# Performance work log

Hardware: AMD Instinct MI355X
Metric: run time of the kernel (lower is better)

## Reference

```python
import jax, jax.numpy as jnp
import numpy as np

DIM = 2048
N_HEADS = 16
N_KV_HEADS = 8
HEAD_DIM = DIM // N_HEADS  # 128
N_REP = N_HEADS // N_KV_HEADS
THETA = 10000.0


def _rope_cos_sin(seq_len, head_dim):
    # freqs_cis = polar(1, outer(t, 1/theta^(2i/d))), i in [0, head_dim//2)
    inv = 1.0 / (THETA ** (jnp.arange(0, head_dim, 2, dtype=jnp.float32) / head_dim))
    t = jnp.arange(seq_len, dtype=jnp.float32)
    freqs = jnp.outer(t, inv)  # [S, hd/2]
    return jnp.cos(freqs), jnp.sin(freqs)


def _apply_rope(x, cos, sin):
    # x: [B, S, H, hd]; pairs (even, odd) treated as complex and multiplied by e^{i*freq}
    xr = x[..., 0::2]
    xi = x[..., 1::2]
    c = cos[None, :, None, :]
    s = sin[None, :, None, :]
    out_r = xr * c - xi * s
    out_i = xr * s + xi * c
    return jnp.stack([out_r, out_i], axis=-1).reshape(x.shape)


def setup_inputs() -> dict:
    key = jax.random.key(0)
    ks = jax.random.split(key, 5)
    B, S = 2, 2048
    sc = 0.02
    return {
        "x": jax.random.normal(ks[0], (B, S, DIM), dtype=jnp.float32),
        "wq": jax.random.normal(ks[1], (N_HEADS * HEAD_DIM, DIM), dtype=jnp.float32) * sc,
        "wk": jax.random.normal(ks[2], (N_KV_HEADS * HEAD_DIM, DIM), dtype=jnp.float32) * sc,
        "wv": jax.random.normal(ks[3], (N_KV_HEADS * HEAD_DIM, DIM), dtype=jnp.float32) * sc,
        "wo": jax.random.normal(ks[4], (DIM, N_HEADS * HEAD_DIM), dtype=jnp.float32) * sc,
        "start_pos": 0,
        "inference": 0,
    }


def reference(x, wq, wk, wv, wo, start_pos, inference):
    B, S, _ = x.shape
    xq = (x @ wq.T).reshape(B, S, N_HEADS, HEAD_DIM)
    xk = (x @ wk.T).reshape(B, S, N_KV_HEADS, HEAD_DIM)
    xv = (x @ wv.T).reshape(B, S, N_KV_HEADS, HEAD_DIM)

    cos, sin = _rope_cos_sin(S, HEAD_DIM)
    xq = _apply_rope(xq, cos, sin)
    xk = _apply_rope(xk, cos, sin)

    # repeat_kv (GQA): [B,S,Hkv,hd] -> [B,S,Hkv*n_rep,hd]
    xk = jnp.repeat(xk, N_REP, axis=2)
    xv = jnp.repeat(xv, N_REP, axis=2)

    q = xq.transpose(0, 2, 1, 3)  # [B,H,S,hd]
    k = xk.transpose(0, 2, 1, 3)
    v = xv.transpose(0, 2, 1, 3)

    scores = jnp.einsum("bhqd,bhkd->bhqk", q, k) / np.sqrt(HEAD_DIM).astype(np.float32)
    mask = jnp.triu(jnp.full((S, S), -jnp.inf, dtype=scores.dtype), k=1)
    scores = scores + mask
    probs = jax.nn.softmax(scores.astype(jnp.float32), axis=-1).astype(q.dtype)

    out = jnp.einsum("bhqk,bhkd->bhqd", probs, v)
    out = out.transpose(0, 2, 1, 3).reshape(B, S, N_HEADS * HEAD_DIM)
    return out @ wo.T
```

## Files before the change

kernel.cpp:

```cpp
#include <hip/hip_runtime.h>
#include <hip/hip_bf16.h>
#include <stdint.h>
#include <type_traits>

typedef __attribute__((ext_vector_type(4))) float   f32x4;
typedef __attribute__((ext_vector_type(8))) __bf16  bf16x8;
typedef __attribute__((ext_vector_type(4))) unsigned int u32x4;

#define B_   2
#define S_   2048
#define DIM_ 2048
#define NH_  16
#define NKV_ 8
#define HD_  128

__device__ inline unsigned short f2bf(float f) {
    unsigned u = __float_as_uint(f);
    unsigned r = (u + 0x7fffu + ((u >> 16) & 1u)) >> 16;
    return (unsigned short)r;
}
__device__ inline float bf2f(unsigned short s) {
    return __uint_as_float(((unsigned)s) << 16);
}

__global__ void k_convert(const float* __restrict__ x,  const float* __restrict__ wq,
                          const float* __restrict__ wk, const float* __restrict__ wv,
                          const float* __restrict__ wo,
                          unsigned short* __restrict__ xb,  unsigned short* __restrict__ wqkb,
                          unsigned short* __restrict__ wvb, unsigned short* __restrict__ wob,
                          float* __restrict__ tab)
{
    int i = blockIdx.x * blockDim.x + threadIdx.x;
    const int NX = 2097152, NWQ = 1048576, NWK = 524288, NWV = 524288, NWO = 1048576;
    const int NTOT = NX + NWQ + NWK + NWV + NWO;
    if (i >= NTOT) {
        int t = i - NTOT;
        if (t >= S_ * 64) return;
        int ii = t & 63;
        int s = t >> 6;
        float inv = expf(-((float)ii / 64.0f) * 9.210340371976184f);
        float ang = (float)s * inv;
        tab[2 * t]     = cosf(ang);
        tab[2 * t + 1] = sinf(ang);
        return;
    }
    const float* src; unsigned short* dst; int j = i;
    if (j < NX) { src = x; dst = xb; }
    else {
        j -= NX;
        if (j < NWQ) { src = wq; dst = wqkb; }
        else {
            j -= NWQ;
            if (j < NWK) { src = wk; dst = wqkb + (size_t)2048 * 2048; }
            else {
                j -= NWK;
                if (j < NWV) { src = wv; dst = wvb; }
                else { j -= NWV; src = wo; dst = wob; }
            }
        }
    }
    float4 v = reinterpret_cast<const float4*>(src)[j];
    ushort4 o;
    o.x = f2bf(v.x); o.y = f2bf(v.y); o.z = f2bf(v.z); o.w = f2bf(v.w);
    reinterpret_cast<ushort4*>(dst)[j] = o;
}

#define BAR  __builtin_amdgcn_s_barrier()
#define WLG  asm volatile("s_waitcnt lgkmcnt(0)" ::: "memory")
#define WVM4 asm volatile("s_waitcnt vmcnt(4)" ::: "memory")
#define WVM6 asm volatile("s_waitcnt vmcnt(6)" ::: "memory")
#define WVM0 asm volatile("s_waitcnt vmcnt(0)" ::: "memory")

#define G_LDS(SRC, DST) __builtin_amdgcn_global_load_lds( \
    (const __attribute__((address_space(1))) void*)(SRC), \
    (__attribute__((address_space(3))) void*)(DST), 16, 0, 0)

#define STAGE(MATB, DBUF, HALF, KT) do { \
    const unsigned short* _s0 = ((MATB) ? pb0 : pa0) + (size_t)(HALF) * 128 * 2048 + (KT) * 64; \
    const unsigned short* _s1 = ((MATB) ? pb1 : pa1) + (size_t)(HALF) * 128 * 2048 + (KT) * 64; \
    G_LDS(_s0, lds + (MATB) * 32768 + (DBUF) * 16384 + (HALF) * 8192 + lo0); \
    G_LDS(_s1, lds + (MATB) * 32768 + (DBUF) * 16384 + (HALF) * 8192 + lo1); \
} while (0)

#define LDA(DBUF, MH) { \
    _Pragma("unroll") \
    for (int mf = 0; mf < 4; ++mf) { \
        _Pragma("unroll") \
        for (int kk = 0; kk < 2; ++kk) { \
            const int R = wm * 128 + (MH) * 64 + mf * 16 + lr; \
            afr[MH][mf][kk] = *reinterpret_cast<const bf16x8*>( \
                &lds[(DBUF) * 16384 + R * 64 + (((kk * 4 + g) ^ (lr & 7)) * 8)]); \
        } } }

#define LDB(DBUF, NH) { \
    _Pragma("unroll") \
    for (int nf = 0; nf < 2; ++nf) { \
        _Pragma("unroll") \
        for (int kk = 0; kk < 2; ++kk) { \
            const int R = wn * 64 + (NH) * 32 + nf * 16 + lr; \
            bfr[NH][nf][kk] = *reinterpret_cast<const bf16x8*>( \
                &lds[32768 + (DBUF) * 16384 + R * 64 + (((kk * 4 + g) ^ (lr & 7)) * 8)]); \
        } } }

#define MMA(MH, NH) { \
    __builtin_amdgcn_s_setprio(1); \
    _Pragma("unroll") \
    for (int mf = 0; mf < 4; ++mf) { \
        _Pragma("unroll") \
        for (int nf = 0; nf < 2; ++nf) { \
            _Pragma("unroll") \
            for (int kk = 0; kk < 2; ++kk) \
                acc[(MH) * 4 + mf][(NH) * 2 + nf] = __builtin_amdgcn_mfma_f32_16x16x32_bf16( \
                    afr[MH][mf][kk], bfr[NH][nf][kk], acc[(MH) * 4 + mf][(NH) * 2 + nf], 0, 0, 0); \
        } } \
    __builtin_amdgcn_s_setprio(0); }

__global__ __launch_bounds__(512, 2) void k_gemm_qkv(
    const unsigned short* __restrict__ A0g, const unsigned short* __restrict__ B0g,
    const unsigned short* __restrict__ A1g,
    unsigned short* __restrict__ Cq, unsigned short* __restrict__ Cv,
    const float* __restrict__ tab)
{
    __shared__ __attribute__((aligned(16))) unsigned short lds[65536];

    const int tid  = threadIdx.x;
    const int lane = tid & 63;
    const int wid  = tid >> 6;
    const int g    = lane >> 4;
    const int lr   = lane & 15;
    const int wm   = wid >> 2;
    const int wn   = wid & 3;

    const unsigned short *Ag, *Bg;
    int brow, bcol;
    bool isQK = true;
    {
        int swz = (blockIdx.x & 7) * 32 + (blockIdx.x >> 3);
        if (swz < 192) { Ag = A0g; Bg = B0g; brow = (swz / 12) << 8; bcol = (swz % 12) << 8; }
        else { int ix = swz - 192; isQK = false; Ag = A1g; Bg = A0g; brow = (ix >> 4) << 8; bcol = (ix & 15) << 8; }
    }

    const int E0 = wid * 512 + lane * 8;
    const int E1 = E0 + 4096;
    const int r0 = E0 >> 6, r1 = E1 >> 6;
    const int c0 = ((((E0 >> 3) & 7) ^ (r0 & 7)) * 8);
    const int c1 = ((((E1 >> 3) & 7) ^ (r1 & 7)) * 8);
    const unsigned short* pa0 = Ag + (size_t)(brow + r0) * 2048 + c0;
    const unsigned short* pa1 = Ag + (size_t)(brow + r1) * 2048 + c1;
    const unsigned short* pb0 = Bg + (size_t)(bcol + r0) * 2048 + c0;
    const unsigned short* pb1 = Bg + (size_t)(bcol + r1) * 2048 + c1;
    const int lo0 = wid * 512;
    const int lo1 = lo0 + 4096;

    f32x4 acc[8][4] = {};
    bf16x8 afr[2][4][2];
    bf16x8 bfr[2][2][2];

    STAGE(0, 0, 0, 0); STAGE(0, 0, 1, 0); STAGE(1, 0, 0, 0); STAGE(1, 0, 1, 0);
    STAGE(0, 1, 0, 1); STAGE(1, 1, 0, 1);
    WVM0; BAR;

    #pragma unroll 1
    for (int i = 0; i < 16; ++i) {
        const int kt1 = 2 * i + 1;
        int kt2 = 2 * i + 2;  if (kt2 >= 32) kt2 -= 32;
        int kt3 = 2 * i + 3;  if (kt3 >= 32) kt3 -= 32;
        LDA(0, 0); LDB(0, 0);
        STAGE(0, 1, 1, kt1);
        BAR; WLG; MMA(0, 0); BAR;
        LDA(0, 1);
        STAGE(1, 1, 1, kt1);
        BAR; WLG; MMA(1, 0); BAR;
        LDB(0, 1);
        STAGE(1, 0, 0, kt2);
        BAR; WLG; MMA(0, 1); BAR;
        STAGE(0, 0, 0, kt2);
        WVM4;
        BAR; WLG; MMA(1, 1); BAR;
        LDA(1, 0); LDB(1, 0);
        STAGE(0, 0, 1, kt2);
        BAR; WLG; MMA(0, 0); BAR;
        LDA(1, 1);
        STAGE(1, 0, 1, kt2);
        BAR; WLG; MMA(1, 0); BAR;
        LDB(1, 1);
        STAGE(1, 1, 0, kt3);
        BAR; WLG; MMA(0, 1); BAR;
        STAGE(0, 1, 0, kt3);
        WVM4;
        BAR; WLG; MMA(1, 1); BAR;
    }

    if (isQK) {
        #pragma unroll
        for (int m = 0; m < 8; ++m) {
            #pragma unroll
            for (int n = 0; n < 4; ++n) {
                int col = bcol + wn * 64 + (n >> 1) * 32 + (n & 1) * 16 + lr;
                int ci  = (col & 127) >> 1;
                int row0 = brow + wm * 128 + (m >> 2) * 64 + (m & 3) * 16 + g * 4;
                #pragma unroll
                for (int r = 0; r < 4; ++r) {
                    int row = row0 + r;
                    int s   = row & (S_ - 1);
                    float2 cs = *reinterpret_cast<const float2*>(&tab[(s * 64 + ci) * 2]);
                    float v = acc[m][n][r];
                    float o = __shfl_xor(v, 1);
                    float res = (lane & 1) ? fmaf(o, cs.y, v * cs.x)
                                           : fmaf(v, cs.x, -(o * cs.y));
                    Cq[(size_t)row * 3072 + col] = f2bf(res);
                }
            }
        }
    } else {
        #pragma unroll
        for (int m = 0; m < 8; ++m)
            #pragma unroll
            for (int n = 0; n < 4; ++n)
                #pragma unroll
                for (int r = 0; r < 4; ++r) {
                    int row = brow + wm * 128 + (m >> 2) * 64 + (m & 3) * 16 + g * 4 + r;
                    int col = bcol + wn * 64 + (n >> 1) * 32 + (n & 1) * 16 + lr;
                    Cv[(size_t)row * 4096 + col] = f2bf(acc[m][n][r]);
                }
    }
}

#define OP_LDA(D, MH) { \
    _Pragma("unroll") \
    for (int mf = 0; mf < 2; ++mf) { \
        _Pragma("unroll") \
        for (int kk = 0; kk < 2; ++kk) { \
            const int R = wm * 64 + (MH) * 32 + mf * 16 + lr; \
            afr[mf][kk] = *reinterpret_cast<const bf16x8*>( \
                &lds[(D) * 8192 + R * 64 + (((kk * 4 + g) ^ (lr & 7)) * 8)]); \
        } } }

#define OP_LDB(D, NH, BFR) { \
    _Pragma("unroll") \
    for (int nf = 0; nf < 2; ++nf) { \
        _Pragma("unroll") \
        for (int kk = 0; kk < 2; ++kk) { \
            const int R = wn * 64 + (NH) * 32 + nf * 16 + lr; \
            BFR[nf][kk] = *reinterpret_cast<const bf16x8*>( \
                &lds[16384 + (D) * 16384 + R * 64 + (((kk * 4 + g) ^ (lr & 7)) * 8)]); \
        } } }

#define OP_MMA(MH, NH, BFR) { \
    __builtin_amdgcn_s_setprio(1); \
    _Pragma("unroll") \
    for (int mf = 0; mf < 2; ++mf) { \
        _Pragma("unroll") \
        for (int nf = 0; nf < 2; ++nf) { \
            _Pragma("unroll") \
            for (int kk = 0; kk < 2; ++kk) \
                acc[(MH) * 2 + mf][(NH) * 2 + nf] = __builtin_amdgcn_mfma_f32_16x16x32_bf16( \
                    afr[mf][kk], BFR[nf][kk], acc[(MH) * 2 + mf][(NH) * 2 + nf], 0, 0, 0); \
        } } \
    __builtin_amdgcn_s_setprio(0); }

#define OP_SA(D, KT) do { \
    G_LDS(pa0 + (KT) * 64, lds + (D) * 8192 + t8); \
    G_LDS(pa1 + (KT) * 64, lds + (D) * 8192 + 4096 + t8); \
} while (0)
#define OP_SB01(D, KT) do { \
    G_LDS(pb0 + (KT) * 64, lds + 16384 + (D) * 16384 + t8); \
    G_LDS(pb1 + (KT) * 64, lds + 16384 + (D) * 16384 + 4096 + t8); \
} while (0)
#define OP_SB23(D, KT) do { \
    G_LDS(pb2 + (KT) * 64, lds + 16384 + (D) * 16384 + 8192 + t8); \
    G_LDS(pb3 + (KT) * 64, lds + 16384 + (D) * 16384 + 12288 + t8); \
} while (0)

__global__ __launch_bounds__(512, 1) void k_gemm_op(
    const unsigned short* __restrict__ Ag,
    const unsigned short* __restrict__ Bg,
    float* __restrict__ C)
{
    __shared__ __attribute__((aligned(16))) unsigned short lds[49152];

    const int tid  = threadIdx.x;
    const int lane = tid & 63;
    const int wid  = tid >> 6;
    const int g    = lane >> 4;
    const int lr   = lane & 15;
    const int wm   = wid >> 2;
    const int wn   = wid & 3;

    const int swz  = (blockIdx.x & 7) * 32 + (blockIdx.x >> 3);
    const int brow = (swz >> 3) << 7;
    const int bcol = (swz & 7) << 8;

    const int E = tid * 8;
    const int r = E >> 6;
    const int c = (((E >> 3) & 7) ^ (r & 7)) * 8;
    const int t8 = tid * 8;
    const unsigned short* pa0 = Ag + (size_t)(brow + r)       * 2048 + c;
    const unsigned short* pa1 = Ag + (size_t)(brow + 64 + r)  * 2048 + c;
    const unsigned short* pb0 = Bg + (size_t)(bcol + r)       * 2048 + c;
    const unsigned short* pb1 = Bg + (size_t)(bcol + 64 + r)  * 2048 + c;
    const unsigned short* pb2 = Bg + (size_t)(bcol + 128 + r) * 2048 + c;
    const unsigned short* pb3 = Bg + (size_t)(bcol + 192 + r) * 2048 + c;

    f32x4 acc[4][4] = {};
    bf16x8 afr[2][2];
    bf16x8 bfr0[2][2], bfr1[2][2];

    OP_SA(0, 0); OP_SB01(0, 0); OP_SB23(0, 0);
    OP_SA(1, 1); OP_SB01(1, 1); OP_SB23(1, 1);
    WVM0; BAR;

    #pragma unroll 1
    for (int i = 0; i < 16; ++i) {
        int kt2 = 2 * i + 2;  if (kt2 >= 32) kt2 -= 32;
        int kt3 = 2 * i + 3;  if (kt3 >= 32) kt3 -= 32;
        OP_LDA(0, 0); OP_LDB(0, 0, bfr0);
        BAR; WLG; OP_MMA(0, 0, bfr0); BAR;
        OP_LDB(0, 1, bfr1);
        BAR; WLG; OP_MMA(0, 1, bfr1); BAR;
        OP_LDA(0, 1);
        OP_SB01(0, kt2);
        BAR; WLG; OP_MMA(1, 0, bfr0); BAR;
        OP_SB23(0, kt2); OP_SA(0, kt2);
        WVM6;
        BAR; WLG; OP_MMA(1, 1, bfr1); BAR;
        OP_LDA(1, 0); OP_LDB(1, 0, bfr0);
        BAR; WLG; OP_MMA(0, 0, bfr0); BAR;
        OP_LDB(1, 1, bfr1);
        BAR; WLG; OP_MMA(0, 1, bfr1); BAR;
        OP_LDA(1, 1);
        OP_SB01(1, kt3);
        BAR; WLG; OP_MMA(1, 0, bfr0); BAR;
        OP_SB23(1, kt3); OP_SA(1, kt3);
        WVM6;
        BAR; WLG; OP_MMA(1, 1, bfr1); BAR;
    }

    #pragma unroll
    for (int m = 0; m < 4; ++m)
        #pragma unroll
        for (int n = 0; n < 4; ++n)
            #pragma unroll
            for (int rr = 0; rr < 4; ++rr) {
                int row = brow + wm * 64 + m * 16 + g * 4 + rr;
                int col = bcol + wn * 64 + n * 16 + lr;
                C[(size_t)row * 2048 + col] = acc[m][n][rr];
            }
}

__global__ __launch_bounds__(512, 4) void k_attn(
    const unsigned short* __restrict__ QK,
    const unsigned short* __restrict__ Vt,
    unsigned short* __restrict__ O)
{
    __shared__ __attribute__((aligned(16))) unsigned short Ks[64 * 128];
    __shared__ __attribute__((aligned(16))) unsigned short Vs[128 * 64];

    const int tid  = threadIdx.x;
    const int lane = tid & 63;
    const int wid  = tid >> 6;
    const int g    = lane >> 4;
    const int lr   = lane & 15;

    const int bid  = blockIdx.x;
    const int hk   = bid & 7;
    const int j    = bid >> 3;
    const int p    = j & 1;
    const int cc   = j >> 1;
    const int h    = (hk << 1) | p;
    const int b    = j >> 5;
    const int base = (cc < 16) ? cc : (31 - cc);
    const int qt   = p ? (15 - base) : base;
    const int q0w  = qt * 128 + wid * 16;

    bf16x8 qf[4];
    #pragma unroll
    for (int c = 0; c < 4; ++c)
        qf[c] = *reinterpret_cast<const bf16x8*>(
            QK + (size_t)(b * S_ + q0w + lr) * 3072 + h * HD_ + c * 32 + g * 8);

    f32x4 o_acc[8] = {};
    float m_run = -INFINITY;
    float l_run = 0.f;

    const float C2 = 1.4426950408889634f * 0.08838834764831845f;
    const int nt = 2 * qt + 2;
    const int srcb = (g & 1) * 32 + lr;
    const bool hig = g >> 1;

    #pragma unroll 1
    for (int t = 0; t < nt; ++t) {
        const int kv0 = t * 64;
        __syncthreads();
        #pragma unroll
        for (int i4 = 0; i4 < 2; ++i4) {
            const int base2 = (i4 * 8 + wid) * 512;
            const int E = base2 + lane * 8;
            {
                int row = E >> 7, ch = (E >> 3) & 15;
                int col = ((ch ^ (row & 15)) * 8);
                G_LDS(QK + (size_t)(b * S_ + kv0 + row) * 3072 + 2048 + hk * HD_ + col,
                      &Ks[base2]);
            }
            {
                int d = E >> 6, ch = (E >> 3) & 7;
                int kv = ((ch ^ (d & 7)) * 8);
                G_LDS(Vt + (size_t)(hk * HD_ + d) * (B_ * S_) + b * S_ + kv0 + kv,
                      &Vs[base2]);
            }
        }
        __syncthreads();

        const bool active = kv0 < q0w + 16;
        if (active) {
            f32x4 sv[4] = {};
            __builtin_amdgcn_s_setprio(1);
            #pragma unroll
            for (int c = 0; c < 4; ++c)
                #pragma unroll
                for (int kvb = 0; kvb < 4; ++kvb) {
                    bf16x8 kf = *reinterpret_cast<const bf16x8*>(
                        &Ks[(kvb * 16 + lr) * 128 + (((c * 4 + g) ^ lr) * 8)]);
                    sv[kvb] = __builtin_amdgcn_mfma_f32_16x16x32_bf16(
                        kf, qf[c], sv[kvb], 0, 0, 0);
                }
            __builtin_amdgcn_s_setprio(0);

            if (kv0 + 63 > q0w) {
                int qg = q0w + lr;
                #pragma unroll
                for (int kvb = 0; kvb < 4; ++kvb) {
                    int kvg0 = kv0 + kvb * 16 + g * 4;
                    #pragma unroll
                    for (int r = 0; r < 4; ++r)
                        if (kvg0 + r > qg) sv[kvb][r] = -INFINITY;
                }
            }

            float m0 = fmaxf(fmaxf(fmaxf(sv[0][0], sv[0][1]), fmaxf(sv[0][2], sv[0][3])),
                             fmaxf(fmaxf(sv[1][0], sv[1][1]), fmaxf(sv[1][2], sv[1][3])));
            m0 = fmaxf(m0, fmaxf(fmaxf(sv[2][0], sv[2][1]), fmaxf(sv[2][2], sv[2][3])));
            m0 = fmaxf(m0, fmaxf(fmaxf(sv[3][0], sv[3][1]), fmaxf(sv[3][2], sv[3][3])));
            m0 = fmaxf(m0, __shfl_xor(m0, 16));
            m0 = fmaxf(m0, __shfl_xor(m0, 32));

            if (__any(m0 > m_run + 90.5f)) {
                float mn = fmaxf(m_run, m0);
                float al = exp2f((m_run - mn) * C2);
                m_run = mn;
                l_run *= al;
                #pragma unroll
                for (int db = 0; db < 8; ++db)
                    #pragma unroll
                    for (int r = 0; r < 4; ++r)
                        o_acc[db][r] *= al;
            }

            unsigned pk[4][2];
            float mb2 = m_run * C2;
            float rs = 0.f;
            #pragma unroll
            for (int kvb = 0; kvb < 4; ++kvb) {
                float p0 = exp2f(fmaf(sv[kvb][0], C2, -mb2));
                float p1 = exp2f(fmaf(sv[kvb][1], C2, -mb2));
                float p2 = exp2f(fmaf(sv[kvb][2], C2, -mb2));
                float p3 = exp2f(fmaf(sv[kvb][3], C2, -mb2));
                rs += (p0 + p1) + (p2 + p3);
                pk[kvb][0] = (unsigned)f2bf(p0) | ((unsigned)f2bf(p1) << 16);
                pk[kvb][1] = (unsigned)f2bf(p2) | ((unsigned)f2bf(p3) << 16);
            }
            rs += __shfl_xor(rs, 16);
            rs += __shfl_xor(rs, 32);
            l_run += rs;

            #pragma unroll
            for (int kk = 0; kk < 2; ++kk) {
                u32x4 w;
                unsigned a0 = (unsigned)__shfl((int)pk[2 * kk][0], srcb);
                unsigned a1 = (unsigned)__shfl((int)pk[2 * kk][1], srcb);
                unsigned a2 = (unsigned)__shfl((int)pk[2 * kk][0], srcb + 16);
                unsigned a3 = (unsigned)__shfl((int)pk[2 * kk][1], srcb + 16);
                unsigned b0 = (unsigned)__shfl((int)pk[2 * kk + 1][0], srcb);
                unsigned b1 = (unsigned)__shfl((int)pk[2 * kk + 1][1], srcb);
                unsigned b2 = (unsigned)__shfl((int)pk[2 * kk + 1][0], srcb + 16);
                unsigned b3 = (unsigned)__shfl((int)pk[2 * kk + 1][1], srcb + 16);
                w[0] = hig ? b0 : a0;
                w[1] = hig ? b1 : a1;
                w[2] = hig ? b2 : a2;
                w[3] = hig ? b3 : a3;
                bf16x8 pb = *reinterpret_cast<const bf16x8*>(&w);
                __builtin_amdgcn_s_setprio(1);
                #pragma unroll
                for (int db = 0; db < 8; ++db) {
                    bf16x8 vf = *reinterpret_cast<const bf16x8*>(
                        &Vs[(db * 16 + lr) * 64 + (((kk * 4 + g) ^ (lr & 7)) * 8)]);
                    o_acc[db] = __builtin_amdgcn_mfma_f32_16x16x32_bf16(
                        vf, pb, o_acc[db], 0, 0, 0);
                }
                __builtin_amdgcn_s_setprio(0);
            }
        }
    }

    {
        float inv = 1.f / l_run;
        size_t rowb = ((size_t)(b * S_ + q0w + lr) * NH_ + h) * HD_;
        #pragma unroll
        for (int db = 0; db < 8; ++db) {
            ushort4 o4;
            o4.x = f2bf(o_acc[db][0] * inv);
            o4.y = f2bf(o_acc[db][1] * inv);
            o4.z = f2bf(o_acc[db][2] * inv);
            o4.w = f2bf(o_acc[db][3] * inv);
            *reinterpret_cast<ushort4*>(&O[rowb + db * 16 + g * 4]) = o4;
        }
    }
}

extern "C" void kernel_launch(void* const* d_in, const int* in_sizes, int n_in,
                              void* d_out, int out_size, void* d_ws, size_t ws_size,
                              hipStream_t stream)
{
    const float* x  = (const float*)d_in[0];
    const float* wq = (const float*)d_in[1];
    const float* wk = (const float*)d_in[2];
    const float* wv = (const float*)d_in[3];
    const float* wo = (const float*)d_in[4];
    float* out = (float*)d_out;

    char* ws = (char*)d_ws;
    size_t off = 0;
    auto alloc = [&](size_t bytes) -> void* {
        void* p = ws + off;
        off += (bytes + 255) & ~(size_t)255;
        return p;
    };
    unsigned short* xb   = (unsigned short*)alloc((size_t)B_ * S_ * DIM_ * 2);
    unsigned short* wqkb = (unsigned short*)alloc((size_t)3072 * 2048 * 2);
    unsigned short* wvb  = (unsigned short*)alloc((size_t)1024 * 2048 * 2);
    unsigned short* wob  = (unsigned short*)alloc((size_t)DIM_ * DIM_ * 2);
    unsigned short* QKb  = (unsigned short*)alloc((size_t)B_ * S_ * 3072 * 2);
    unsigned short* Vtb  = (unsigned short*)alloc((size_t)1024 * B_ * S_ * 2);
    unsigned short* Ob   = (unsigned short*)alloc((size_t)B_ * S_ * NH_ * HD_ * 2);
    float* tab = (float*)alloc((size_t)S_ * 64 * 2 * 4);

    k_convert<<<20992, 256, 0, stream>>>(x, wq, wk, wv, wo, xb, wqkb, wvb, wob, tab);
    k_gemm_qkv<<<256, 512, 0, stream>>>(xb, wqkb, wvb, QKb, Vtb, tab);
    k_attn<<<B_ * NH_ * (S_ / 128), 512, 0, stream>>>(QKb, Vtb, Ob);
    k_gemm_op<<<256, 512, 0, stream>>>(Ob, wob, out);

    (void)in_sizes; (void)n_in; (void)out_size; (void)ws_size;
}
```

Before: 209.1 us.

## Double-buffer K/V tiles in attention kernel to overlap loads with MFMA

Splits the K and V shared-memory tiles into two buffers. The next KV tile is issued via direct global-to-LDS loads while the current tile is computed, using partial vmcnt waits and barriers. This aims to hide global load latency behind the QK and PV matrix multiplies. It doubles LDS use per block, which may reduce the number of resident blocks per CU.

```diff
diff --git a/kernel.cpp b/kernel.cpp
--- a/kernel.cpp
+++ b/kernel.cpp
@@ -353,8 +353,8 @@
     const unsigned short* __restrict__ Vt,
     unsigned short* __restrict__ O)
 {
-    __shared__ __attribute__((aligned(16))) unsigned short Ks[64 * 128];
-    __shared__ __attribute__((aligned(16))) unsigned short Vs[128 * 64];
+    __shared__ __attribute__((aligned(16))) unsigned short Ks[2][64 * 128];
+    __shared__ __attribute__((aligned(16))) unsigned short Vs[2][128 * 64];
 
     const int tid  = threadIdx.x;
     const int lane = tid & 63;
@@ -365,12 +365,12 @@
     const int bid  = blockIdx.x;
     const int hk   = bid & 7;
     const int j    = bid >> 3;
-    const int p    = j & 1;
+    const int p_   = j & 1;
     const int cc   = j >> 1;
-    const int h    = (hk << 1) | p;
+    const int h    = (hk << 1) | p_;
     const int b    = j >> 5;
     const int base = (cc < 16) ? cc : (31 - cc);
-    const int qt   = p ? (15 - base) : base;
+    const int qt   = p_ ? (15 - base) : base;
     const int q0w  = qt * 128 + wid * 16;
 
     bf16x8 qf[4];
@@ -388,28 +388,36 @@
     const int srcb = (g & 1) * 32 + lr;
     const bool hig = g >> 1;
 
+#define ATTN_STAGE(T, P) do { \
+    const int kv0s = (T) * 64; \
+    _Pragma("unroll") \
+    for (int i4 = 0; i4 < 2; ++i4) { \
+        const int base2 = (i4 * 8 + wid) * 512; \
+        const int E = base2 + lane * 8; \
+        { int row = E >> 7, ch = (E >> 3) & 15; \
+          int col = ((ch ^ (row & 15)) * 8); \
+          G_LDS(QK + (size_t)(b * S_ + kv0s + row) * 3072 + 2048 + hk * HD_ + col, \
+                &Ks[P][base2]); } \
+        { int d = E >> 6, ch = (E >> 3) & 7; \
+          int kv = ((ch ^ (d & 7)) * 8); \
+          G_LDS(Vt + (size_t)(hk * HD_ + d) * (B_ * S_) + b * S_ + kv0s + kv, \
+                &Vs[P][base2]); } \
+    } \
+} while (0)
+
+    ATTN_STAGE(0, 0);
+
     #pragma unroll 1
     for (int t = 0; t < nt; ++t) {
+        const int p = t & 1;
         const int kv0 = t * 64;
-        __syncthreads();
-        #pragma unroll
-        for (int i4 = 0; i4 < 2; ++i4) {
-            const int base2 = (i4 * 8 + wid) * 512;
-            const int E = base2 + lane * 8;
-            {
-                int row = E >> 7, ch = (E >> 3) & 15;
-                int col = ((ch ^ (row & 15)) * 8);
-                G_LDS(QK + (size_t)(b * S_ + kv0 + row) * 3072 + 2048 + hk * HD_ + col,
-                      &Ks[base2]);
-            }
-            {
-                int d = E >> 6, ch = (E >> 3) & 7;
-                int kv = ((ch ^ (d & 7)) * 8);
-                G_LDS(Vt + (size_t)(hk * HD_ + d) * (B_ * S_) + b * S_ + kv0 + kv,
-                      &Vs[base2]);
-            }
+        if (t + 1 < nt) {
+            ATTN_STAGE(t + 1, p ^ 1);
+            WVM4;
+        } else {
+            WVM0;
         }
-        __syncthreads();
+        BAR;
 
         const bool active = kv0 < q0w + 16;
         if (active) {
@@ -420,7 +428,7 @@
                 #pragma unroll
                 for (int kvb = 0; kvb < 4; ++kvb) {
                     bf16x8 kf = *reinterpret_cast<const bf16x8*>(
-                        &Ks[(kvb * 16 + lr) * 128 + (((c * 4 + g) ^ lr) * 8)]);
+                        &Ks[p][(kvb * 16 + lr) * 128 + (((c * 4 + g) ^ lr) * 8)]);
                     sv[kvb] = __builtin_amdgcn_mfma_f32_16x16x32_bf16(
                         kf, qf[c], sv[kvb], 0, 0, 0);
                 }
@@ -493,13 +501,14 @@
                 #pragma unroll
                 for (int db = 0; db < 8; ++db) {
                     bf16x8 vf = *reinterpret_cast<const bf16x8*>(
-                        &Vs[(db * 16 + lr) * 64 + (((kk * 4 + g) ^ (lr & 7)) * 8)]);
+                        &Vs[p][(db * 16 + lr) * 64 + (((kk * 4 + g) ^ (lr & 7)) * 8)]);
                     o_acc[db] = __builtin_amdgcn_mfma_f32_16x16x32_bf16(
                         vf, pb, o_acc[db], 0, 0, 0);
                 }
                 __builtin_amdgcn_s_setprio(0);
             }
         }
+        BAR;
     }
 
     {
@@ -515,6 +524,7 @@
             *reinterpret_cast<ushort4*>(&O[rowb + db * 16 + g * 4]) = o4;
         }
     }
+#undef ATTN_STAGE
 }
 
 extern "C" void kernel_launch(void* const* d_in, const int* in_sizes, int n_in,
```

Measured after the change: 208.8 us. About the same (-0.1%).

## Split attention KV range in two and merge partials in a combine kernel

Applied to the files above, without the earlier changes.

Each attention query tile now runs as two blocks, each covering half of the causal KV range, which doubles the grid to 1024 blocks and halves the per-block serial loop. Unnormalized partial outputs in bf16 plus per-row (max, sum) are written into reused workspace buffers. A new combine kernel merges them with log-sum-exp weights and writes the normalized output. Launch bounds are raised to 8 blocks per CU. The split adds an extra kernel launch, extra global traffic, and an extra bf16 rounding of the partials.

```diff
diff --git a/kernel.cpp b/kernel.cpp
--- a/kernel.cpp
+++ b/kernel.cpp
@@ -348,10 +348,11 @@
             }
 }
 
-__global__ __launch_bounds__(512, 4) void k_attn(
+__global__ __launch_bounds__(512, 8) void k_attn(
     const unsigned short* __restrict__ QK,
     const unsigned short* __restrict__ Vt,
-    unsigned short* __restrict__ O)
+    unsigned short* __restrict__ Opart,
+    float2* __restrict__ Ml)
 {
     __shared__ __attribute__((aligned(16))) unsigned short Ks[64 * 128];
     __shared__ __attribute__((aligned(16))) unsigned short Vs[128 * 64];
@@ -364,13 +365,15 @@
 
     const int bid  = blockIdx.x;
     const int hk   = bid & 7;
-    const int j    = bid >> 3;
-    const int p    = j & 1;
-    const int cc   = j >> 1;
-    const int h    = (hk << 1) | p;
-    const int b    = j >> 5;
+    const int jj   = bid >> 3;
+    const int half = jj & 1;
+    const int j2   = jj >> 1;
+    const int p_   = j2 & 1;
+    const int cc   = j2 >> 1;
+    const int h    = (hk << 1) | p_;
+    const int b    = j2 >> 5;
     const int base = (cc < 16) ? cc : (31 - cc);
-    const int qt   = p ? (15 - base) : base;
+    const int qt   = p_ ? (15 - base) : base;
     const int q0w  = qt * 128 + wid * 16;
 
     bf16x8 qf[4];
@@ -384,12 +387,13 @@
     float l_run = 0.f;
 
     const float C2 = 1.4426950408889634f * 0.08838834764831845f;
-    const int nt = 2 * qt + 2;
+    const int t0 = half * (qt + 1);
+    const int t1 = t0 + qt + 1;
     const int srcb = (g & 1) * 32 + lr;
     const bool hig = g >> 1;
 
     #pragma unroll 1
-    for (int t = 0; t < nt; ++t) {
+    for (int t = t0; t < t1; ++t) {
         const int kv0 = t * 64;
         __syncthreads();
         #pragma unroll
@@ -503,18 +507,56 @@
     }
 
     {
-        float inv = 1.f / l_run;
-        size_t rowb = ((size_t)(b * S_ + q0w + lr) * NH_ + h) * HD_;
+        const int slot = (((b * 16 + h) * 16 + qt) * 2) + half;
+        const size_t obase = (size_t)slot * 128 * 128 + (size_t)(wid * 16 + lr) * 128;
         #pragma unroll
         for (int db = 0; db < 8; ++db) {
             ushort4 o4;
-            o4.x = f2bf(o_acc[db][0] * inv);
-            o4.y = f2bf(o_acc[db][1] * inv);
-            o4.z = f2bf(o_acc[db][2] * inv);
-            o4.w = f2bf(o_acc[db][3] * inv);
-            *reinterpret_cast<ushort4*>(&O[rowb + db * 16 + g * 4]) = o4;
+            o4.x = f2bf(o_acc[db][0]);
+            o4.y = f2bf(o_acc[db][1]);
+            o4.z = f2bf(o_acc[db][2]);
+            o4.w = f2bf(o_acc[db][3]);
+            *reinterpret_cast<ushort4*>(&Opart[obase + db * 16 + g * 4]) = o4;
         }
-    }
+        if (lane < 16)
+            Ml[slot * 128 + wid * 16 + lr] = make_float2(m_run, l_run);
+    }
+}
+
+__global__ __launch_bounds__(256) void k_combine(
+    const unsigned short* __restrict__ Opart,
+    const float2* __restrict__ Ml,
+    unsigned short* __restrict__ Ob)
+{
+    const int gt  = blockIdx.x * 256 + threadIdx.x;
+    const int u   = gt >> 12;
+    const int rem = gt & 4095;
+    const int rr  = rem >> 5;
+    const int dq  = rem & 31;
+
+    const float C2 = 1.4426950408889634f * 0.08838834764831845f;
+    const float2 ml0 = Ml[(u * 2) * 128 + rr];
+    const float2 ml1 = Ml[(u * 2 + 1) * 128 + rr];
+    const float m  = fmaxf(ml0.x, ml1.x);
+    const float w0 = exp2f((ml0.x - m) * C2);
+    const float w1 = exp2f((ml1.x - m) * C2);
+    const float inv = 1.f / fmaf(w0, ml0.y, w1 * ml1.y);
+
+    const ushort4 a = *reinterpret_cast<const ushort4*>(
+        &Opart[((size_t)(u * 2) * 128 + rr) * 128 + dq * 4]);
+    const ushort4 c = *reinterpret_cast<const ushort4*>(
+        &Opart[((size_t)(u * 2 + 1) * 128 + rr) * 128 + dq * 4]);
+    ushort4 o;
+    o.x = f2bf(fmaf(w0, bf2f(a.x), w1 * bf2f(c.x)) * inv);
+    o.y = f2bf(fmaf(w0, bf2f(a.y), w1 * bf2f(c.y)) * inv);
+    o.z = f2bf(fmaf(w0, bf2f(a.z), w1 * bf2f(c.z)) * inv);
+    o.w = f2bf(fmaf(w0, bf2f(a.w), w1 * bf2f(c.w)) * inv);
+
+    const int b  = u >> 8;
+    const int h  = (u >> 4) & 15;
+    const int qt = u & 15;
+    *reinterpret_cast<ushort4*>(
+        &Ob[((size_t)(b * S_ + qt * 128 + rr) * NH_ + h) * HD_ + dq * 4]) = o;
 }
 
 extern "C" void kernel_launch(void* const* d_in, const int* in_sizes, int n_in,
@@ -544,9 +586,13 @@
     unsigned short* Ob   = (unsigned short*)alloc((size_t)B_ * S_ * NH_ * HD_ * 2);
     float* tab = (float*)alloc((size_t)S_ * 64 * 2 * 4);
 
+    unsigned short* Opart = xb;
+    float2*         Ml    = (float2*)tab;
+
     k_convert<<<20992, 256, 0, stream>>>(x, wq, wk, wv, wo, xb, wqkb, wvb, wob, tab);
     k_gemm_qkv<<<256, 512, 0, stream>>>(xb, wqkb, wvb, QKb, Vtb, tab);
-    k_attn<<<B_ * NH_ * (S_ / 128), 512, 0, stream>>>(QKb, Vtb, Ob);
+    k_attn<<<1024, 512, 0, stream>>>(QKb, Vtb, Opart, Ml);
+    k_combine<<<8192, 256, 0, stream>>>(Opart, Ml, Ob);
     k_gemm_op<<<256, 512, 0, stream>>>(Ob, wob, out);
 
     (void)in_sizes; (void)n_in; (void)out_size; (void)ws_size;
```

Result: slower. 414.4 us (+98.2%).
